# Kernel tuning notes

Hardware: AMD Instinct MI355X
Metric: run time of the kernel (lower is better)

## Reference

```python
import jax, jax.numpy as jnp
import numpy as np

D = 1024
H = 16
DH = D // H  # 64


def setup_inputs() -> dict:
    key = jax.random.key(0)
    ks = jax.random.split(key, 7)
    X = jax.random.normal(ks[0], (2, 2048, D), dtype=jnp.float32)
    # Per-head projection weights stacked along head axis: [H, D, DH]
    s = 1.0 / np.sqrt(D)
    Wq = jax.random.uniform(ks[1], (H, D, DH), jnp.float32, -s, s)
    Wk = jax.random.uniform(ks[2], (H, D, DH), jnp.float32, -s, s)
    Wv = jax.random.uniform(ks[3], (H, D, DH), jnp.float32, -s, s)
    bq = jax.random.uniform(ks[4], (H, DH), jnp.float32, -s, s)
    bk = jax.random.uniform(ks[5], (H, DH), jnp.float32, -s, s)
    bv = jax.random.uniform(ks[6], (H, DH), jnp.float32, -s, s)
    return {"X": X, "Wq": Wq, "bq": bq, "Wk": Wk, "bk": bk, "Wv": Wv, "bv": bv}


def reference(X, Wq, bq, Wk, bk, Wv, bv):
    B, S, _ = X.shape
    # Per-head linear projections (batched over heads): [B, H, S, DH]
    Q = jnp.einsum('bsd,hde->bhse', X, Wq) + bq[None, :, None, :]
    K = jnp.einsum('bsd,hde->bhse', X, Wk) + bk[None, :, None, :]
    V = jnp.einsum('bsd,hde->bhse', X, Wv) + bv[None, :, None, :]
    scale = jnp.sqrt(jnp.asarray(DH, dtype=X.dtype))
    QK = jnp.einsum('bhse,bhte->bhst', Q, K) / scale  # [B, H, S, S]
    # Faithful to source: softmax over full row FIRST, then lower-tri mask
    # (post-softmax tril, no renormalization).
    sQK = jax.nn.softmax(QK, axis=-1)
    tril = jnp.tril(jnp.ones((S, S), dtype=X.dtype))
    sQK = sQK * tril
    out = jnp.einsum('bhst,bhte->bhse', sQK, V)  # [B, H, S, DH]
    # Concatenate heads along feature dim (torch.cat over per-head outputs)
    return out.transpose(0, 2, 1, 3).reshape(B, S, H * DH)
```

## Files before the change

### kernel.cpp

```cpp
#include <hip/hip_runtime.h>
#include <math.h>

#define B_  2
#define S_  2048
#define D_  1024
#define H_  16
#define DH_ 64

typedef unsigned short u16;
typedef unsigned int   u32;
typedef _Float16       f16;
typedef _Float16 half8  __attribute__((ext_vector_type(8)));
typedef _Float16 half4  __attribute__((ext_vector_type(4)));
typedef float    f32x4  __attribute__((ext_vector_type(4)));

#if __has_builtin(__builtin_amdgcn_exp2f)
#define EXP2(x) __builtin_amdgcn_exp2f(x)
#else
#define EXP2(x) exp2f(x)
#endif

__device__ __forceinline__ uint4 ld_u4(const u16* p){
    const u32* q = (const u32*)p;
    uint4 r; r.x = q[0]; r.y = q[1]; r.z = q[2]; r.w = q[3];
    return r;
}
__device__ __forceinline__ void st_u4(u16* p, uint4 v){
    u32* q = (u32*)p;
    q[0] = v.x; q[1] = v.y; q[2] = v.z; q[3] = v.w;
}
__device__ __forceinline__ u16 h_bits(f16 h){ return __builtin_bit_cast(u16, h); }

__global__ __launch_bounds__(256) void convert_w_kernel(
    const float* __restrict__ Wq, const float* __restrict__ Wk,
    const float* __restrict__ Wv, u16* __restrict__ Wt)
{
    __shared__ float Wf[64][65];
    const int c  = threadIdx.x;
    const int d0 = blockIdx.x * 64;
    const int h  = blockIdx.y;
    const int which = blockIdx.z;
    const float* src = (which == 0) ? Wq : (which == 1) ? Wk : Wv;
    src += (size_t)h * D_ * DH_;

    #pragma unroll
    for (int it = 0; it < 4; ++it){
        int d  = (c >> 4) + 16 * it;
        int e4 = (c & 15) * 4;
        float4 v = *(const float4*)(src + (size_t)(d0 + d) * DH_ + e4);
        Wf[d][e4+0] = v.x; Wf[d][e4+1] = v.y; Wf[d][e4+2] = v.z; Wf[d][e4+3] = v.w;
    }
    __syncthreads();
    u16* dst = Wt + (size_t)(which * H_ + h) * DH_ * D_;
    #pragma unroll
    for (int it = 0; it < 4; ++it){
        int e  = (c >> 4) + 16 * it;
        int d4 = (c & 15) * 4;
        u16 q[4];
        #pragma unroll
        for (int j = 0; j < 4; ++j)
            q[j] = h_bits((f16)(Wf[d4 + j][e] * 64.0f));
        u32* p = (u32*)(dst + (size_t)e * D_ + d0 + d4);
        p[0] = q[0] | ((u32)q[1] << 16);
        p[1] = q[2] | ((u32)q[3] << 16);
    }
}

#define PKS 34

__global__ __launch_bounds__(256, 3) void proj_kernel(
    const float* __restrict__ X, const u16* __restrict__ Wt,
    const float* __restrict__ bq, const float* __restrict__ bk,
    const float* __restrict__ bv,
    f16* __restrict__ Qh, f16* __restrict__ Kh, f16* __restrict__ Vh)
{
    __shared__ u16 XsHi[128 * PKS], XsLo[128 * PKS], Bs[128 * PKS];

    const int tid  = threadIdx.x;
    const int lane = tid & 63;
    const int w    = tid >> 6;
    const int quad = lane >> 4;
    const int ln   = lane & 15;
    const int wr   = (w >> 1) * 64;
    const int wc   = (w & 1) * 64;
    const int m0   = blockIdx.x * 128;
    const int c0   = blockIdx.y * 128;

    f32x4 acc[4][4];
    #pragma unroll
    for (int i = 0; i < 4; ++i)
        #pragma unroll
        for (int j = 0; j < 4; ++j)
            acc[i][j] = (f32x4){0.f, 0.f, 0.f, 0.f};

    for (int k0 = 0; k0 < D_; k0 += 32){
        __syncthreads();
        #pragma unroll
        for (int it = 0; it < 4; ++it){
            int idx = tid + 256 * it;
            int r   = idx >> 3;
            int ch  = (idx & 7) * 4;
            float4 v = *(const float4*)(X + (size_t)(m0 + r) * D_ + k0 + ch);
            float fv[4] = {v.x, v.y, v.z, v.w};
            u16 hh[4], ll[4];
            #pragma unroll
            for (int j = 0; j < 4; ++j){
                f16 hi = (f16)fv[j];
                hh[j] = h_bits(hi);
                ll[j] = h_bits((f16)(fv[j] - (float)hi));
            }
            u32* ph = (u32*)&XsHi[r * PKS + ch];
            ph[0] = hh[0] | ((u32)hh[1] << 16);
            ph[1] = hh[2] | ((u32)hh[3] << 16);
            u32* pl = (u32*)&XsLo[r * PKS + ch];
            pl[0] = ll[0] | ((u32)ll[1] << 16);
            pl[1] = ll[2] | ((u32)ll[3] << 16);
        }
        #pragma unroll
        for (int it = 0; it < 2; ++it){
            int idx = tid + 256 * it;
            int col = idx >> 2;
            int ch  = (idx & 3) * 8;
            st_u4(&Bs[col * PKS + ch],
                  *(const uint4*)(Wt + (size_t)(c0 + col) * D_ + k0 + ch));
        }
        __syncthreads();

        half8 ahi[4], alo[4], bf[4];
        #pragma unroll
        for (int mt = 0; mt < 4; ++mt){
            int row = wr + 16 * mt + ln;
            ahi[mt] = __builtin_bit_cast(half8, ld_u4(&XsHi[row * PKS + quad * 8]));
            alo[mt] = __builtin_bit_cast(half8, ld_u4(&XsLo[row * PKS + quad * 8]));
        }
        #pragma unroll
        for (int nt = 0; nt < 4; ++nt)
            bf[nt] = __builtin_bit_cast(half8,
                ld_u4(&Bs[(wc + 16 * nt + ln) * PKS + quad * 8]));
        #pragma unroll
        for (int mt = 0; mt < 4; ++mt)
            #pragma unroll
            for (int nt = 0; nt < 4; ++nt){
                acc[mt][nt] = __builtin_amdgcn_mfma_f32_16x16x32_f16(ahi[mt], bf[nt], acc[mt][nt], 0, 0, 0);
                acc[mt][nt] = __builtin_amdgcn_mfma_f32_16x16x32_f16(alo[mt], bf[nt], acc[mt][nt], 0, 0, 0);
            }
    }

    const float QSCALE = 0.125f * 1.44269504088896340736f;
    const float INV64  = 0.015625f;
    #pragma unroll
    for (int nt = 0; nt < 4; ++nt){
        int colg  = c0 + wc + 16 * nt + ln;
        int which = colg >> 10;
        int h     = (colg >> 6) & 15;
        int e     = colg & 63;
        const float* bp = (which == 0) ? bq : (which == 1) ? bk : bv;
        f16* op = (which == 0) ? Qh : (which == 1) ? Kh : Vh;
        float bias  = bp[h * DH_ + e];
        float scale = (which == 0) ? QSCALE : 1.0f;
        #pragma unroll
        for (int mt = 0; mt < 4; ++mt)
            #pragma unroll
            for (int r = 0; r < 4; ++r){
                int sg = m0 + wr + 16 * mt + 4 * quad + r;
                int b  = sg >> 11;
                int s  = sg & (S_ - 1);
                float val = (acc[mt][nt][r] * INV64 + bias) * scale;
                op[((size_t)(b * H_ + h) * S_ + s) * DH_ + e] = (f16)val;
            }
    }
}

__global__ __launch_bounds__(256) void transpose_v_kernel(
    const f16* __restrict__ Vh, f16* __restrict__ Vt)
{
    __shared__ u16 T[64 * 70];
    const int c  = threadIdx.x;
    const int t0 = blockIdx.x * 64;
    const int bh = blockIdx.y;
    const u16* src = (const u16*)Vh + (size_t)bh * S_ * DH_;
    #pragma unroll
    for (int it = 0; it < 2; ++it){
        int idx = c + 256 * it;
        int t  = idx >> 3;
        int ch = (idx & 7) * 8;
        st_u4(&T[t * 70 + ch], *(const uint4*)(src + (size_t)(t0 + t) * DH_ + ch));
    }
    __syncthreads();
    u16* dst = (u16*)Vt + (size_t)bh * DH_ * S_;
    #pragma unroll
    for (int it = 0; it < 2; ++it){
        int idx = c + 256 * it;
        int e  = idx >> 3;
        int tg = (idx & 7) * 8;
        u16 v[8];
        #pragma unroll
        for (int j = 0; j < 8; ++j) v[j] = T[(tg + j) * 70 + e];
        uint4 u;
        u.x = v[0] | ((u32)v[1] << 16);
        u.y = v[2] | ((u32)v[3] << 16);
        u.z = v[4] | ((u32)v[5] << 16);
        u.w = v[6] | ((u32)v[7] << 16);
        *(uint4*)(dst + (size_t)e * S_ + t0 + tg) = u;
    }
}

#define AKS 72

__global__ __launch_bounds__(256, 4) void attn_kernel(
    const f16* __restrict__ Qh, const f16* __restrict__ Kh,
    const f16* __restrict__ Vt, float* __restrict__ Out)
{
    __shared__ u16 Ks[64 * AKS];
    __shared__ u16 Vs[64 * AKS];

    const int tid  = threadIdx.x;
    const int lane = tid & 63;
    const int w    = tid >> 6;
    const int quad = lane >> 4;
    const int ln   = lane & 15;
    const int i    = blockIdx.x;
    const int h    = blockIdx.y;
    const int b    = blockIdx.z;
    const int bh   = b * H_ + h;
    const int sub  = w & 1;
    const int qbase = (w >> 1) ? (S_ - 32 * (i + 1) + 16 * sub)
                               : (32 * i + 16 * sub);
    const int vmax  = S_ - 32 * i - 1;

    const u16* Qg = (const u16*)Qh + (size_t)bh * S_ * DH_;
    const u16* Kg = (const u16*)Kh + (size_t)bh * S_ * DH_;
    const u16* Vg = (const u16*)Vt + (size_t)bh * DH_ * S_;

    half8 qf[2];
    #pragma unroll
    for (int ks = 0; ks < 2; ++ks)
        qf[ks] = __builtin_bit_cast(half8,
            *(const uint4*)(Qg + (size_t)(qbase + ln) * DH_ + 32 * ks + 8 * quad));

    const int kr = tid >> 3;
    const int kc = (tid & 7) * 8;

    uint4 kA = *(const uint4*)(Kg + (size_t)kr * DH_ + kc);
    uint4 kB = *(const uint4*)(Kg + (size_t)(kr + 32) * DH_ + kc);
    uint4 vA = *(const uint4*)(Vg + (size_t)kr * S_ + kc);
    uint4 vB = *(const uint4*)(Vg + (size_t)(kr + 32) * S_ + kc);

    float l_r = 0.f;
    f32x4 o_acc[4];
    #pragma unroll
    for (int nt = 0; nt < 4; ++nt) o_acc[nt] = (f32x4){0.f, 0.f, 0.f, 0.f};

    const int qrow   = qbase + ln;
    const int pv_lim = qbase + 15;

    for (int t0 = 0; t0 < S_; t0 += 64){
        __syncthreads();
        *(uint4*)&Ks[kr * AKS + kc]        = kA;
        *(uint4*)&Ks[(kr + 32) * AKS + kc] = kB;
        if (t0 <= vmax){
            *(uint4*)&Vs[kr * AKS + kc]        = vA;
            *(uint4*)&Vs[(kr + 32) * AKS + kc] = vB;
        }
        const int tn = t0 + 64;
        if (tn < S_){
            kA = *(const uint4*)(Kg + (size_t)(tn + kr) * DH_ + kc);
            kB = *(const uint4*)(Kg + (size_t)(tn + kr + 32) * DH_ + kc);
            if (tn <= vmax){
                vA = *(const uint4*)(Vg + (size_t)kr * S_ + tn + kc);
                vB = *(const uint4*)(Vg + (size_t)(kr + 32) * S_ + tn + kc);
            }
        }
        __syncthreads();

        f32x4 sc[4];
        #pragma unroll
        for (int mt = 0; mt < 4; ++mt) sc[mt] = (f32x4){0.f, 0.f, 0.f, 0.f};
        #pragma unroll
        for (int ks = 0; ks < 2; ++ks)
            #pragma unroll
            for (int mt = 0; mt < 4; ++mt){
                half8 kf = __builtin_bit_cast(half8,
                    *(const uint4*)&Ks[(16 * mt + ln) * AKS + 32 * ks + 8 * quad]);
                sc[mt] = __builtin_amdgcn_mfma_f32_16x16x32_f16(kf, qf[ks], sc[mt], 0, 0, 0);
            }

        #pragma unroll
        for (int mt = 0; mt < 4; ++mt)
            #pragma unroll
            for (int r = 0; r < 4; ++r)
                sc[mt][r] = EXP2(sc[mt][r]);
        float s = ((sc[0][0] + sc[0][1] + sc[0][2] + sc[0][3]) +
                   (sc[1][0] + sc[1][1] + sc[1][2] + sc[1][3])) +
                  ((sc[2][0] + sc[2][1] + sc[2][2] + sc[2][3]) +
                   (sc[3][0] + sc[3][1] + sc[3][2] + sc[3][3]));
        s += __shfl_xor(s, 16);
        s += __shfl_xor(s, 32);
        l_r += s;

        if (t0 <= pv_lim){
            half4 pf[4];
            #pragma unroll
            for (int mt = 0; mt < 4; ++mt){
                int tb = t0 + 16 * mt + 4 * quad;
                #pragma unroll
                for (int r = 0; r < 4; ++r)
                    pf[mt][r] = (tb + r > qrow) ? (f16)0.f : (f16)sc[mt][r];
            }
            #pragma unroll
            for (int nt = 0; nt < 4; ++nt)
                #pragma unroll
                for (int mt = 0; mt < 4; ++mt){
                    half4 vf = __builtin_bit_cast(half4,
                        *(const uint2*)&Vs[(16 * nt + ln) * AKS + 16 * mt + 4 * quad]);
                    o_acc[nt] = __builtin_amdgcn_mfma_f32_16x16x16f16(pf[mt], vf, o_acc[nt], 0, 0, 0);
                }
        }
    }

    #pragma unroll
    for (int r = 0; r < 4; ++r){
        float lv  = __shfl(l_r, (lane & 48) | (4 * quad + r));
        float inv = 1.0f / lv;
        int sg = qbase + 4 * quad + r;
        float* op = Out + ((size_t)b * S_ + sg) * D_ + h * DH_;
        #pragma unroll
        for (int nt = 0; nt < 4; ++nt)
            op[16 * nt + ln] = o_acc[nt][r] * inv;
    }
}

extern "C" void kernel_launch(void* const* d_in, const int* in_sizes, int n_in,
                              void* d_out, int out_size, void* d_ws, size_t ws_size,
                              hipStream_t stream)
{
    const float* X  = (const float*)d_in[0];
    const float* Wq = (const float*)d_in[1];
    const float* bq = (const float*)d_in[2];
    const float* Wk = (const float*)d_in[3];
    const float* bk = (const float*)d_in[4];
    const float* Wv = (const float*)d_in[5];
    const float* bv = (const float*)d_in[6];
    float* out = (float*)d_out;

    u16* Wt = (u16*)d_ws;
    f16* Qh = (f16*)(Wt + 3145728);
    f16* Kh = Qh + 4194304;
    f16* Vh = Kh + 4194304;
    f16* Vt = Vh + 4194304;

    convert_w_kernel<<<dim3(16, 16, 3), 256, 0, stream>>>(Wq, Wk, Wv, Wt);
    proj_kernel<<<dim3(32, 24), 256, 0, stream>>>(X, Wt, bq, bk, bv, Qh, Kh, Vh);
    transpose_v_kernel<<<dim3(32, 32), 256, 0, stream>>>(Vh, Vt);
    attn_kernel<<<dim3(32, 16, 2), 256, 0, stream>>>(Qh, Kh, Vt, out);
}
```

Before: 207.6 us.

## Pre-split X into fp16 hi/lo and register-prefetch tiles in projection GEMM

Adds a separate kernel that splits X into fp16 high and low halves once, instead of every projection block column redoing the conversion (24x redundant). The projection GEMM now loads pre-split fp16 tiles with 16-byte vector loads and prefetches the next k-tile into registers while computing the current one. LDS padding changes to 40 so 16-byte shared stores and loads stay aligned. In exchange it adds an extra kernel launch, extra global traffic for the hi/lo buffers, and more registers held for the prefetch. Vt now aliases the Xhi workspace region, which is safe only because proj finishes before transpose_v writes Vt.

```diff
diff --git a/kernel.cpp b/kernel.cpp
--- a/kernel.cpp
+++ b/kernel.cpp
@@ -20,16 +20,33 @@
 #define EXP2(x) exp2f(x)
 #endif
 
-__device__ __forceinline__ uint4 ld_u4(const u16* p){
-    const u32* q = (const u32*)p;
-    uint4 r; r.x = q[0]; r.y = q[1]; r.z = q[2]; r.w = q[3];
-    return r;
-}
 __device__ __forceinline__ void st_u4(u16* p, uint4 v){
     u32* q = (u32*)p;
     q[0] = v.x; q[1] = v.y; q[2] = v.z; q[3] = v.w;
 }
 __device__ __forceinline__ u16 h_bits(f16 h){ return __builtin_bit_cast(u16, h); }
+
+__global__ __launch_bounds__(256) void split_x_kernel(
+    const float* __restrict__ X, u16* __restrict__ Xhi, u16* __restrict__ Xlo)
+{
+    const int idx = blockIdx.x * 256 + threadIdx.x;
+    float4 v = ((const float4*)X)[idx];
+    float fv[4] = {v.x, v.y, v.z, v.w};
+    u16 hh[4], ll[4];
+    #pragma unroll
+    for (int j = 0; j < 4; ++j){
+        f16 hi = (f16)fv[j];
+        hh[j] = h_bits(hi);
+        ll[j] = h_bits((f16)(fv[j] - (float)hi));
+    }
+    uint2 ph, pl;
+    ph.x = hh[0] | ((u32)hh[1] << 16);
+    ph.y = hh[2] | ((u32)hh[3] << 16);
+    pl.x = ll[0] | ((u32)ll[1] << 16);
+    pl.y = ll[2] | ((u32)ll[3] << 16);
+    ((uint2*)Xhi)[idx] = ph;
+    ((uint2*)Xlo)[idx] = pl;
+}
 
 __global__ __launch_bounds__(256) void convert_w_kernel(
     const float* __restrict__ Wq, const float* __restrict__ Wk,
@@ -66,10 +83,11 @@
     }
 }
 
-#define PKS 34
+#define PKS 40
 
 __global__ __launch_bounds__(256, 3) void proj_kernel(
-    const float* __restrict__ X, const u16* __restrict__ Wt,
+    const u16* __restrict__ Xhi, const u16* __restrict__ Xlo,
+    const u16* __restrict__ Wt,
     const float* __restrict__ bq, const float* __restrict__ bk,
     const float* __restrict__ bv,
     f16* __restrict__ Qh, f16* __restrict__ Kh, f16* __restrict__ Vh)
@@ -86,6 +104,20 @@
     const int m0   = blockIdx.x * 128;
     const int c0   = blockIdx.y * 128;
 
+    const int sr  = tid >> 2;
+    const int sch = (tid & 3) * 8;
+
+    const u16* xh0 = Xhi + (size_t)(m0 + sr) * D_ + sch;
+    const u16* xh1 = xh0 + (size_t)64 * D_;
+    const u16* xl0 = Xlo + (size_t)(m0 + sr) * D_ + sch;
+    const u16* xl1 = xl0 + (size_t)64 * D_;
+    const u16* wb0 = Wt  + (size_t)(c0 + sr) * D_ + sch;
+    const u16* wb1 = wb0 + (size_t)64 * D_;
+
+    uint4 rh0 = *(const uint4*)xh0, rh1 = *(const uint4*)xh1;
+    uint4 rl0 = *(const uint4*)xl0, rl1 = *(const uint4*)xl1;
+    uint4 rw0 = *(const uint4*)wb0, rw1 = *(const uint4*)wb1;
+
     f32x4 acc[4][4];
     #pragma unroll
     for (int i = 0; i < 4; ++i)
@@ -95,34 +127,17 @@
 
     for (int k0 = 0; k0 < D_; k0 += 32){
         __syncthreads();
-        #pragma unroll
-        for (int it = 0; it < 4; ++it){
-            int idx = tid + 256 * it;
-            int r   = idx >> 3;
-            int ch  = (idx & 7) * 4;
-            float4 v = *(const float4*)(X + (size_t)(m0 + r) * D_ + k0 + ch);
-            float fv[4] = {v.x, v.y, v.z, v.w};
-            u16 hh[4], ll[4];
-            #pragma unroll
-            for (int j = 0; j < 4; ++j){
-                f16 hi = (f16)fv[j];
-                hh[j] = h_bits(hi);
-                ll[j] = h_bits((f16)(fv[j] - (float)hi));
-            }
-            u32* ph = (u32*)&XsHi[r * PKS + ch];
-            ph[0] = hh[0] | ((u32)hh[1] << 16);
-            ph[1] = hh[2] | ((u32)hh[3] << 16);
-            u32* pl = (u32*)&XsLo[r * PKS + ch];
-            pl[0] = ll[0] | ((u32)ll[1] << 16);
-            pl[1] = ll[2] | ((u32)ll[3] << 16);
-        }
-        #pragma unroll
-        for (int it = 0; it < 2; ++it){
-            int idx = tid + 256 * it;
-            int col = idx >> 2;
-            int ch  = (idx & 3) * 8;
-            st_u4(&Bs[col * PKS + ch],
-                  *(const uint4*)(Wt + (size_t)(c0 + col) * D_ + k0 + ch));
+        *(uint4*)&XsHi[sr * PKS + sch]        = rh0;
+        *(uint4*)&XsHi[(sr + 64) * PKS + sch] = rh1;
+        *(uint4*)&XsLo[sr * PKS + sch]        = rl0;
+        *(uint4*)&XsLo[(sr + 64) * PKS + sch] = rl1;
+        *(uint4*)&Bs[sr * PKS + sch]          = rw0;
+        *(uint4*)&Bs[(sr + 64) * PKS + sch]   = rw1;
+        const int kn = k0 + 32;
+        if (kn < D_){
+            rh0 = *(const uint4*)(xh0 + kn); rh1 = *(const uint4*)(xh1 + kn);
+            rl0 = *(const uint4*)(xl0 + kn); rl1 = *(const uint4*)(xl1 + kn);
+            rw0 = *(const uint4*)(wb0 + kn); rw1 = *(const uint4*)(wb1 + kn);
         }
         __syncthreads();
 
@@ -130,13 +145,13 @@
         #pragma unroll
         for (int mt = 0; mt < 4; ++mt){
             int row = wr + 16 * mt + ln;
-            ahi[mt] = __builtin_bit_cast(half8, ld_u4(&XsHi[row * PKS + quad * 8]));
-            alo[mt] = __builtin_bit_cast(half8, ld_u4(&XsLo[row * PKS + quad * 8]));
+            ahi[mt] = __builtin_bit_cast(half8, *(const uint4*)&XsHi[row * PKS + quad * 8]);
+            alo[mt] = __builtin_bit_cast(half8, *(const uint4*)&XsLo[row * PKS + quad * 8]);
         }
         #pragma unroll
         for (int nt = 0; nt < 4; ++nt)
             bf[nt] = __builtin_bit_cast(half8,
-                ld_u4(&Bs[(wc + 16 * nt + ln) * PKS + quad * 8]));
+                *(const uint4*)&Bs[(wc + 16 * nt + ln) * PKS + quad * 8]);
         #pragma unroll
         for (int mt = 0; mt < 4; ++mt)
             #pragma unroll
@@ -343,14 +358,17 @@
     const float* bv = (const float*)d_in[6];
     float* out = (float*)d_out;
 
-    u16* Wt = (u16*)d_ws;
-    f16* Qh = (f16*)(Wt + 3145728);
-    f16* Kh = Qh + 4194304;
-    f16* Vh = Kh + 4194304;
-    f16* Vt = Vh + 4194304;
-
+    u16* Wt  = (u16*)d_ws;
+    f16* Qh  = (f16*)(Wt + 3145728);
+    f16* Kh  = Qh + 4194304;
+    f16* Vh  = Kh + 4194304;
+    u16* Xhi = (u16*)(Vh + 4194304);
+    u16* Xlo = Xhi + 4194304;
+    f16* Vt  = (f16*)Xhi;
+
+    split_x_kernel<<<dim3(4096), 256, 0, stream>>>(X, Xhi, Xlo);
     convert_w_kernel<<<dim3(16, 16, 3), 256, 0, stream>>>(Wq, Wk, Wv, Wt);
-    proj_kernel<<<dim3(32, 24), 256, 0, stream>>>(X, Wt, bq, bk, bv, Qh, Kh, Vh);
+    proj_kernel<<<dim3(32, 24), 256, 0, stream>>>(Xhi, Xlo, Wt, bq, bk, bv, Qh, Kh, Vh);
     transpose_v_kernel<<<dim3(32, 32), 256, 0, stream>>>(Vh, Vt);
     attn_kernel<<<dim3(32, 16, 2), 256, 0, stream>>>(Qh, Kh, Vt, out);
 }
```

After: 203.9 us. About the same (-1.8%).
